# Optimization experiments

Measured on AMD Instinct MI355X. Metric: run time of the kernel, lower is better.

The kernel has to match this reference:

```python
import jax, jax.numpy as jnp
import numpy as np

EPS = 1e-8
ROUTING_ITERS = 3

def squash(t, axis=-1):
    sq = jnp.sum(t * t, axis=axis, keepdims=True)
    scale = sq / (1.0 + sq)
    return scale * t / jnp.sqrt(sq + EPS)

def setup_inputs() -> dict:
    key = jax.random.key(0)
    k1, k2 = jax.random.split(key)
    B, R, C, D_out, D_in = 512, 1152, 10, 16, 8
    x = jax.random.normal(k1, (B, R, D_in), dtype=jnp.float32)
    W = jax.random.normal(k2, (R, C, D_out, D_in), dtype=jnp.float32) * 0.01
    return {"x": x, "W": W}

def reference(x, W):
    # u_hat[b,r,c,o] = sum_i W[r,c,o,i] * x[b,r,i]
    u_hat = jnp.einsum('rcoi,bri->brco', W, x)  # (B,R,C,O)
    B, R, C, _ = u_hat.shape
    b_ij = jnp.zeros((B, R, C, 1), dtype=u_hat.dtype)
    v_j = None
    for i in range(ROUTING_ITERS):
        c_ij = jax.nn.softmax(b_ij, axis=2)                 # softmax over classes
        s_j = jnp.sum(c_ij * u_hat, axis=1, keepdims=True)  # (B,1,C,O)
        v_j = squash(s_j, axis=-1)
        if i < ROUTING_ITERS - 1:
            agreement = jnp.sum(u_hat * v_j, axis=-1, keepdims=True)  # (B,R,C,1)
            b_ij = b_ij + agreement
    return jnp.squeeze(v_j, axis=1)  # (B, C, O)
```

## Files before the change

### kernel.cpp

```cpp
#include <hip/hip_runtime.h>
#include <hip/hip_fp16.h>
#include <math.h>


#define R_TOT 1152
#define C_N 10
#define O_N 16
#define I_N 8
#define B_TOT 512
#define RT 64
#define RCHB 18
#define CHUNK 6
#define NCH 3
#define SEG (B_TOT * C_N * O_N)
#define ROWS (C_N * O_N)
#define CGR (CHUNK * ROWS)

typedef _Float16 v8h __attribute__((ext_vector_type(8)));
typedef float v4f __attribute__((ext_vector_type(4)));
typedef unsigned u32x4 __attribute__((ext_vector_type(4)));

__device__ __forceinline__ unsigned packf2(float a, float b) {
  unsigned ua = (unsigned)__half_as_ushort(__float2half(a));
  unsigned ub = (unsigned)__half_as_ushort(__float2half(b));
  return ua | (ub << 16);
}

__device__ __forceinline__ float oreduce(float a) {
#if __has_builtin(__builtin_amdgcn_permlane16_swap) && \
    __has_builtin(__builtin_amdgcn_permlane32_swap)
  typedef unsigned uv2 __attribute__((ext_vector_type(2)));
  unsigned au = __float_as_uint(a);
  uv2 t = __builtin_amdgcn_permlane16_swap(au, au, false, false);
  const float s16 = __uint_as_float(t.x) + __uint_as_float(t.y);
  unsigned su = __float_as_uint(s16);
  uv2 t2 = __builtin_amdgcn_permlane32_swap(su, su, false, false);
  return __uint_as_float(t2.x) + __uint_as_float(t2.y);
#else
  a += __shfl_xor(a, 16);
  a += __shfl_xor(a, 32);
  return a;
#endif
}

template<bool UNIFORM>
__global__ __launch_bounds__(256, 2) void acc_kernel(
    const float* __restrict__ x, const float* __restrict__ W,
    const float* __restrict__ vsum, float* __restrict__ part)
{
  __shared__ uint4 wbuf[2 * CGR];

  const int tid  = threadIdx.x;
  const int wave = tid >> 6;
  const int lane = tid & 63;
  const int bq   = lane & 15;
  const int og   = lane >> 4;
  const bool lo32 = (lane < 32);

  const int bid   = blockIdx.x;
  const int xcd   = bid & 7;
  const int idx   = bid >> 3;
  const int rtile = xcd * 8 + (idx & 7);
  const int btile = idx >> 3;

  const int b  = btile * 64 + wave * 16 + bq;
  const int r0 = rtile * RCHB;
  const int og8 = (og & 1) * 8;

  auto stage = [&](int ci, int buf) {
    const int rbase = r0 + ci * CHUNK;
    #pragma unroll 1
    for (int g = tid; g < CGR; g += 256) {
      const float4* wsrc = reinterpret_cast<const float4*>(W)
                         + ((size_t)rbase * ROWS + g) * 2;
      const float4 a = wsrc[0], c4 = wsrc[1];
      uint4 v;
      v.x = packf2(a.x, a.y);  v.y = packf2(a.z, a.w);
      v.z = packf2(c4.x, c4.y); v.w = packf2(c4.z, c4.w);
      wbuf[buf * CGR + g] = v;
    }
  };

  auto xload = [&](int r) -> uint2 {
    uint2 v; v.x = 0u; v.y = 0u;
    if (lo32) {
      const float4 xv = *reinterpret_cast<const float4*>(
          &x[((size_t)b * R_TOT + r) * I_N + (og & 1) * 4]);
      v.x = packf2(xv.x, xv.y);
      v.y = packf2(xv.z, xv.w);
    }
    return v;
  };

  float vf[C_N][4];
  if constexpr (!UNIFORM) {
    #pragma unroll
    for (int c = 0; c < C_N; ++c) {
      const float4 tv = *reinterpret_cast<const float4*>(
          &vsum[((size_t)b * C_N + c) * O_N + og * 4]);
      vf[c][0] = tv.x; vf[c][1] = tv.y; vf[c][2] = tv.z; vf[c][3] = tv.w;
    }
  }

  float sacc[C_N][4];
  #pragma unroll
  for (int c = 0; c < C_N; ++c)
    #pragma unroll
    for (int j = 0; j < 4; ++j) sacc[c][j] = 0.0f;

  uint2 xc, xn;
  stage(0, 0);
  xc = xload(r0);
  __syncthreads();

  #pragma unroll 1
  for (int ci = 0; ci < NCH; ++ci) {
    if (ci + 1 < NCH) stage(ci + 1, (ci + 1) & 1);
    const int sb = (ci & 1) * CGR;
    #pragma unroll 1
    for (int rr = 0; rr < CHUNK; ++rr) {
      const int rl = ci * CHUNK + rr;
      const int rn = (rl + 1 < RCHB) ? rl + 1 : rl;
      xn = xload(r0 + rn);

      u32x4 bxv = {xc.x, xc.y, 0u, 0u};
      const v8h bf = __builtin_bit_cast(v8h, bxv);
      const char* wb = reinterpret_cast<const char*>(&wbuf[sb + rr * ROWS]);

      float u[C_N][4];
      #pragma unroll
      for (int cg = 0; cg < 2; ++cg) {
        uint2 w8[5];
        #pragma unroll
        for (int c5 = 0; c5 < 5; ++c5) { w8[c5].x = 0u; w8[c5].y = 0u; }
        if (lo32) {
          #pragma unroll
          for (int c5 = 0; c5 < 5; ++c5) {
            const int c = cg * 5 + c5;
            w8[c5] = *reinterpret_cast<const uint2*>(
                wb + (c * 16 + bq) * 16 + og8);
          }
        }
        #pragma unroll
        for (int c5 = 0; c5 < 5; ++c5) {
          u32x4 axv = {w8[c5].x, w8[c5].y, 0u, 0u};
          v4f d = __builtin_amdgcn_mfma_f32_16x16x32_f16(
              __builtin_bit_cast(v8h, axv), bf,
              (v4f){0.f, 0.f, 0.f, 0.f}, 0, 0, 0);
          const int c = cg * 5 + c5;
          u[c][0] = d[0]; u[c][1] = d[1]; u[c][2] = d[2]; u[c][3] = d[3];
        }
      }

      if constexpr (UNIFORM) {
        #pragma unroll
        for (int c = 0; c < C_N; ++c)
          #pragma unroll
          for (int j = 0; j < 4; ++j) sacc[c][j] += u[c][j];
      } else {
        float bij[C_N];
        #pragma unroll
        for (int c = 0; c < C_N; ++c) {
          const float a = u[c][0] * vf[c][0] + u[c][1] * vf[c][1]
                        + u[c][2] * vf[c][2] + u[c][3] * vf[c][3];
          bij[c] = oreduce(a);
        }
        float m = bij[0];
        #pragma unroll
        for (int c = 1; c < C_N; ++c) m = fmaxf(m, bij[c]);
        float e[C_N];
        float den = 0.0f;
        #pragma unroll
        for (int c = 0; c < C_N; ++c) { e[c] = __expf(bij[c] - m); den += e[c]; }
        const float inv = __builtin_amdgcn_rcpf(den);
        #pragma unroll
        for (int c = 0; c < C_N; ++c) {
          const float cw = e[c] * inv;
          #pragma unroll
          for (int j = 0; j < 4; ++j) sacc[c][j] += cw * u[c][j];
        }
      }
      xc = xn;
    }
    __syncthreads();
  }

  const float scale = UNIFORM ? 0.1f : 1.0f;
  float* pb = part + (size_t)rtile * SEG;
  #pragma unroll
  for (int c = 0; c < C_N; ++c) {
    float4 v;
    v.x = sacc[c][0] * scale; v.y = sacc[c][1] * scale;
    v.z = sacc[c][2] * scale; v.w = sacc[c][3] * scale;
    *reinterpret_cast<float4*>(
        &pb[((size_t)b * C_N + c) * O_N + og * 4]) = v;
  }
}

template<int MODE>
__global__ __launch_bounds__(256) void reduce_squash(
    const float* __restrict__ part, int nrt,
    float* __restrict__ vsum, float* __restrict__ out)
{
  __shared__ float lds[4][64];
  const int tid = threadIdx.x;
  const int l   = tid & 63;
  const int q   = tid >> 6;
  const int j   = blockIdx.x * 64 + l;
  const float* p = part + j;
  float sv = 0.0f;
  #pragma unroll 4
  for (int rt = q; rt < nrt; rt += 4) sv += p[(size_t)rt * SEG];
  lds[q][l] = sv;
  __syncthreads();
  if (q == 0) {
    sv = lds[0][l] + lds[1][l] + lds[2][l] + lds[3][l];
    float sq = sv * sv;
    sq += __shfl_xor(sq, 1);
    sq += __shfl_xor(sq, 2);
    sq += __shfl_xor(sq, 4);
    sq += __shfl_xor(sq, 8);
    const float scale = sq / (1.0f + sq) * rsqrtf(sq + 1e-8f);
    const float v = scale * sv;
    if constexpr (MODE == 0)      vsum[j] = v;
    else if constexpr (MODE == 1) vsum[j] += v;
    else                          out[j] = v;
  }
}

extern "C" void kernel_launch(void* const* d_in, const int* in_sizes, int n_in,
                              void* d_out, int out_size, void* d_ws, size_t ws_size,
                              hipStream_t stream) {
  (void)in_sizes; (void)n_in; (void)out_size; (void)ws_size;
  const float* x = (const float*)d_in[0];
  const float* W = (const float*)d_in[1];
  float* out  = (float*)d_out;
  float* part = (float*)d_ws;

  const dim3 blk(256), accGrid(8 * RT), sqGrid(SEG / 64);

  hipLaunchKernelGGL((acc_kernel<true>),  accGrid, blk, 0, stream, x, W, out, part);
  hipLaunchKernelGGL((reduce_squash<0>),  sqGrid,  blk, 0, stream, part, RT, out, out);
  hipLaunchKernelGGL((acc_kernel<false>), accGrid, blk, 0, stream, x, W, out, part);
  hipLaunchKernelGGL((reduce_squash<1>),  sqGrid,  blk, 0, stream, part, RT, out, out);
  hipLaunchKernelGGL((acc_kernel<false>), accGrid, blk, 0, stream, x, W, out, part);
  hipLaunchKernelGGL((reduce_squash<2>),  sqGrid,  blk, 0, stream, part, RT, out, out);
}
```

Measured before the change: 104.5 us.

## Software-pipeline MFMA u_hat computation against routing softmax across rows

Restructures the per-row loop into a two-stage software pipeline: u_hat for the next row is computed via MFMA while the routing/softmax accumulation for the current row runs, using ping-pong register arrays. Launch bounds are relaxed to one block per SIMD-group so the extra live registers fit. This aims to hide MFMA and LDS latency behind VALU work, at the cost of higher register pressure and lower occupancy.

```diff
diff --git a/kernel.cpp b/kernel.cpp
--- a/kernel.cpp
+++ b/kernel.cpp
@@ -44,7 +44,7 @@
 }
 
 template<bool UNIFORM>
-__global__ __launch_bounds__(256, 2) void acc_kernel(
+__global__ __launch_bounds__(256, 1) void acc_kernel(
     const float* __restrict__ x, const float* __restrict__ W,
     const float* __restrict__ vsum, float* __restrict__ part)
 {
@@ -81,15 +81,45 @@
     }
   };
 
-  auto xload = [&](int r) -> uint2 {
+  auto xloadc = [&](int rloc) -> uint2 {
+    const int rl = (rloc < RCHB) ? rloc : (RCHB - 1);
     uint2 v; v.x = 0u; v.y = 0u;
     if (lo32) {
       const float4 xv = *reinterpret_cast<const float4*>(
-          &x[((size_t)b * R_TOT + r) * I_N + (og & 1) * 4]);
+          &x[((size_t)b * R_TOT + (r0 + rl)) * I_N + (og & 1) * 4]);
       v.x = packf2(xv.x, xv.y);
       v.y = packf2(xv.z, xv.w);
     }
     return v;
+  };
+
+  auto compute_u = [&](int slabG, uint2 xf, float (&u)[C_N][4]) {
+    u32x4 bxv = {xf.x, xf.y, 0u, 0u};
+    const v8h bfr = __builtin_bit_cast(v8h, bxv);
+    const char* wb = reinterpret_cast<const char*>(&wbuf[slabG]);
+    #pragma unroll
+    for (int cg = 0; cg < 2; ++cg) {
+      uint2 w8[5];
+      #pragma unroll
+      for (int c5 = 0; c5 < 5; ++c5) { w8[c5].x = 0u; w8[c5].y = 0u; }
+      if (lo32) {
+        #pragma unroll
+        for (int c5 = 0; c5 < 5; ++c5) {
+          const int c = cg * 5 + c5;
+          w8[c5] = *reinterpret_cast<const uint2*>(
+              wb + (c * 16 + bq) * 16 + og8);
+        }
+      }
+      #pragma unroll
+      for (int c5 = 0; c5 < 5; ++c5) {
+        u32x4 axv = {w8[c5].x, w8[c5].y, 0u, 0u};
+        v4f d = __builtin_amdgcn_mfma_f32_16x16x32_f16(
+            __builtin_bit_cast(v8h, axv), bfr,
+            (v4f){0.f, 0.f, 0.f, 0.f}, 0, 0, 0);
+        const int c = cg * 5 + c5;
+        u[c][0] = d[0]; u[c][1] = d[1]; u[c][2] = d[2]; u[c][3] = d[3];
+      }
+    }
   };
 
   float vf[C_N][4];
@@ -108,81 +138,68 @@
     #pragma unroll
     for (int j = 0; j < 4; ++j) sacc[c][j] = 0.0f;
 
-  uint2 xc, xn;
+  auto routing = [&](float (&u)[C_N][4]) {
+    if constexpr (UNIFORM) {
+      #pragma unroll
+      for (int c = 0; c < C_N; ++c)
+        #pragma unroll
+        for (int j = 0; j < 4; ++j) sacc[c][j] += u[c][j];
+    } else {
+      float bij[C_N];
+      #pragma unroll
+      for (int c = 0; c < C_N; ++c) {
+        const float a = u[c][0] * vf[c][0] + u[c][1] * vf[c][1]
+                      + u[c][2] * vf[c][2] + u[c][3] * vf[c][3];
+        bij[c] = oreduce(a);
+      }
+      float m = bij[0];
+      #pragma unroll
+      for (int c = 1; c < C_N; ++c) m = fmaxf(m, bij[c]);
+      float e[C_N];
+      float den = 0.0f;
+      #pragma unroll
+      for (int c = 0; c < C_N; ++c) { e[c] = __expf(bij[c] - m); den += e[c]; }
+      const float inv = __builtin_amdgcn_rcpf(den);
+      #pragma unroll
+      for (int c = 0; c < C_N; ++c) {
+        const float cw = e[c] * inv;
+        #pragma unroll
+        for (int j = 0; j < 4; ++j) sacc[c][j] += cw * u[c][j];
+      }
+    }
+  };
+
+  float ua[C_N][4], ub[C_N][4];
   stage(0, 0);
-  xc = xload(r0);
+  uint2 xc = xloadc(0);
   __syncthreads();
+  compute_u(0, xc, ua);
+  xc = xloadc(1);
 
   #pragma unroll 1
   for (int ci = 0; ci < NCH; ++ci) {
     if (ci + 1 < NCH) stage(ci + 1, (ci + 1) & 1);
     const int sb = (ci & 1) * CGR;
     #pragma unroll 1
-    for (int rr = 0; rr < CHUNK; ++rr) {
+    for (int rr = 0; rr < CHUNK; rr += 2) {
       const int rl = ci * CHUNK + rr;
-      const int rn = (rl + 1 < RCHB) ? rl + 1 : rl;
-      xn = xload(r0 + rn);
-
-      u32x4 bxv = {xc.x, xc.y, 0u, 0u};
-      const v8h bf = __builtin_bit_cast(v8h, bxv);
-      const char* wb = reinterpret_cast<const char*>(&wbuf[sb + rr * ROWS]);
-
-      float u[C_N][4];
-      #pragma unroll
-      for (int cg = 0; cg < 2; ++cg) {
-        uint2 w8[5];
-        #pragma unroll
-        for (int c5 = 0; c5 < 5; ++c5) { w8[c5].x = 0u; w8[c5].y = 0u; }
-        if (lo32) {
-          #pragma unroll
-          for (int c5 = 0; c5 < 5; ++c5) {
-            const int c = cg * 5 + c5;
-            w8[c5] = *reinterpret_cast<const uint2*>(
-                wb + (c * 16 + bq) * 16 + og8);
-          }
-        }
-        #pragma unroll
-        for (int c5 = 0; c5 < 5; ++c5) {
-          u32x4 axv = {w8[c5].x, w8[c5].y, 0u, 0u};
-          v4f d = __builtin_amdgcn_mfma_f32_16x16x32_f16(
-              __builtin_bit_cast(v8h, axv), bf,
-              (v4f){0.f, 0.f, 0.f, 0.f}, 0, 0, 0);
-          const int c = cg * 5 + c5;
-          u[c][0] = d[0]; u[c][1] = d[1]; u[c][2] = d[2]; u[c][3] = d[3];
-        }
-      }
-
-      if constexpr (UNIFORM) {
-        #pragma unroll
-        for (int c = 0; c < C_N; ++c)
-          #pragma unroll
-          for (int j = 0; j < 4; ++j) sacc[c][j] += u[c][j];
+      compute_u(sb + (rr + 1) * ROWS, xc, ub);
+      uint2 x2 = xloadc(rl + 2);
+      routing(ua);
+      if (rr + 2 < CHUNK) {
+        compute_u(sb + (rr + 2) * ROWS, x2, ua);
+        xc = xloadc(rl + 3);
+        routing(ub);
       } else {
-        float bij[C_N];
-        #pragma unroll
-        for (int c = 0; c < C_N; ++c) {
-          const float a = u[c][0] * vf[c][0] + u[c][1] * vf[c][1]
-                        + u[c][2] * vf[c][2] + u[c][3] * vf[c][3];
-          bij[c] = oreduce(a);
-        }
-        float m = bij[0];
-        #pragma unroll
-        for (int c = 1; c < C_N; ++c) m = fmaxf(m, bij[c]);
-        float e[C_N];
-        float den = 0.0f;
-        #pragma unroll
-        for (int c = 0; c < C_N; ++c) { e[c] = __expf(bij[c] - m); den += e[c]; }
-        const float inv = __builtin_amdgcn_rcpf(den);
-        #pragma unroll
-        for (int c = 0; c < C_N; ++c) {
-          const float cw = e[c] * inv;
-          #pragma unroll
-          for (int j = 0; j < 4; ++j) sacc[c][j] += cw * u[c][j];
-        }
-      }
-      xc = xn;
+        routing(ub);
+        xc = x2;
+      }
     }
     __syncthreads();
+    if (ci + 1 < NCH) {
+      compute_u(((ci + 1) & 1) * CGR, xc, ua);
+      xc = xloadc((ci + 1) * CHUNK + 1);
+    }
   }
 
   const float scale = UNIFORM ? 0.1f : 1.0f;
```

Result: slower. 136.4 us (+30.6%).
